# Kernel optimization log

Hardware: AMD Instinct MI355X
Metric: run time of the kernel (lower is better)

## Reference

```python
import jax, jax.numpy as jnp
import numpy as np

B, N, D = 32, 128, 1024


def _euclid_cost(a, b):
    # a: [N, D], b: [N, D] -> [N, N] Euclidean distances (torch.cdist p=2)
    a = a.astype(np.float64)
    b = b.astype(np.float64)
    sq = (a * a).sum(-1)[:, None] + (b * b).sum(-1)[None, :] - 2.0 * (a @ b.T)
    return np.sqrt(np.maximum(sq, 0.0))


def _hungarian(cost):
    """Exact LAP via shortest augmenting path (Kuhn-Munkres with potentials).
    Returns col_for_row: row i is matched to column col_for_row[i].
    Equivalent to scipy.optimize.linear_sum_assignment on a square matrix
    (row_ind == arange(N))."""
    n = cost.shape[0]
    INF = 1e18
    c = cost.astype(np.float64)
    u = np.zeros(n + 1)
    v = np.zeros(n + 1)
    p = np.zeros(n + 1, dtype=np.int64)   # p[j] = row matched to column j (1-based)
    way = np.zeros(n + 1, dtype=np.int64)
    for i in range(1, n + 1):
        p[0] = i
        j0 = 0
        minv = np.full(n + 1, INF)
        used = np.zeros(n + 1, dtype=bool)
        while True:
            used[j0] = True
            i0 = p[j0]
            free = ~used[1:]
            cand = c[i0 - 1] - u[i0] - v[1:]
            better = free & (cand < minv[1:])
            idx = np.nonzero(better)[0]
            minv[idx + 1] = cand[idx]
            way[idx + 1] = j0
            free_j = np.nonzero(free)[0] + 1
            j1 = free_j[np.argmin(minv[free_j])]
            delta = minv[j1]
            u[p[used]] += delta
            v[used] -= delta
            minv[~used] -= delta
            j0 = j1
            if p[j0] == 0:
                break
        while j0:
            j1 = way[j0]
            p[j0] = p[j1]
            j0 = j1
    col_for_row = np.zeros(n, dtype=np.int64)
    for j in range(1, n + 1):
        col_for_row[p[j] - 1] = j - 1
    return col_for_row


def _match(pred_nodes, target_nodes):
    # Host-side exact bipartite matching (mirrors the .cpu() + scipy solve;
    # non-differentiable, indices treated as constants like torch's detach()).
    pn = np.asarray(jax.device_get(pred_nodes))
    tn = np.asarray(jax.device_get(target_nodes))
    cols = [_hungarian(_euclid_cost(pn[b], tn[b])) for b in range(pn.shape[0])]
    return jnp.asarray(np.stack(cols))  # [B, N] int64


def setup_inputs() -> dict:
    key = jax.random.key(0)
    k1, k2, k3, k4 = jax.random.split(key, 4)
    return {
        "pred_nodes": jax.random.normal(k1, (B, N, D), dtype=jnp.float32),
        "target_nodes": jax.random.normal(k2, (B, N, D), dtype=jnp.float32),
        "pred_adj": jax.random.normal(k3, (B, N, N), dtype=jnp.float32),
        "target_adj": jax.random.normal(k4, (B, N, N), dtype=jnp.float32),
    }


def reference(pred_nodes, target_nodes, pred_adj, target_adj):
    col = _match(pred_nodes, target_nodes)  # [B, N]; row_ind is identity
    # matched target nodes: target_nodes[b][col_ind]
    tn_m = jnp.take_along_axis(target_nodes, col[:, :, None], axis=1)  # [B, N, D]
    # nn.MSELoss() = mean over elements per sample; losses summed over batch
    node_loss = jnp.mean((pred_nodes - tn_m) ** 2, axis=(1, 2)).sum()
    # target_adj[b][col_ind][:, col_ind]; pred_adj row_ind gather is identity
    ta_m = jnp.take_along_axis(target_adj, col[:, :, None], axis=1)
    ta_m = jnp.take_along_axis(ta_m, col[:, None, :], axis=2)  # [B, N, N]
    edge_loss = jnp.mean((pred_adj - ta_m) ** 2, axis=(1, 2)).sum()
    return node_loss, edge_loss
```

## Files before the change

kernel.cpp:

```cpp
#include <hip/hip_runtime.h>
#include <hip/hip_bf16.h>
#include <math.h>

#define BB 32
#define NN 128
#define DD 1024
#define INF64 1e30

__global__ __launch_bounds__(128) void cost_kernel(const float* __restrict__ pred,
                                                   const float* __restrict__ tgt,
                                                   double* __restrict__ cost) {
  int blk = blockIdx.x;
  int b = blk >> 4;
  int it = (blk & 15) << 3;
  const float* Ab = pred + ((size_t)b * NN + it) * DD;
  const float* Bb = tgt + (size_t)b * NN * DD;
  __shared__ float a_s[8 * DD];
  for (int t = threadIdx.x; t < 8 * DD / 4; t += 128) {
    ((float4*)a_s)[t] = ((const float4*)Ab)[t];
  }
  __syncthreads();
  const int j = threadIdx.x;
  const float4* brow = (const float4*)(Bb + (size_t)j * DD);
  double acc[8];
#pragma unroll
  for (int r = 0; r < 8; r++) acc[r] = 0.0;
  for (int k4 = 0; k4 < DD / 4; k4++) {
    float4 bv = brow[k4];
#pragma unroll
    for (int r = 0; r < 8; r++) {
      float4 av = ((const float4*)(a_s + r * DD))[k4];
      double d0 = (double)av.x - (double)bv.x;
      double d1 = (double)av.y - (double)bv.y;
      double d2 = (double)av.z - (double)bv.z;
      double d3 = (double)av.w - (double)bv.w;
      acc[r] += d0 * d0 + d1 * d1 + d2 * d2 + d3 * d3;
    }
  }
#pragma unroll
  for (int r = 0; r < 8; r++) {
    cost[(((size_t)b * NN) + it + r) * NN + j] = sqrt(acc[r]);
  }
}

union f64u { double d; unsigned int i[2]; };

__device__ __forceinline__ double readlane_f64(double x, int lane) {
  f64u u; u.d = x;
  f64u v;
  v.i[0] = (unsigned)__builtin_amdgcn_readlane((int)u.i[0], lane);
  v.i[1] = (unsigned)__builtin_amdgcn_readlane((int)u.i[1], lane);
  return v.d;
}

__device__ __forceinline__ double readpair_f64(double a, double b, int idx) {
  int l = (idx - 1) & 63;
  double ra = readlane_f64(a, l);
  double rb = readlane_f64(b, l);
  return ((idx - 1) >> 6) ? rb : ra;
}

__device__ __forceinline__ int readpair_i32(int a, int b, int idx) {
  int l = (idx - 1) & 63;
  int ra = __builtin_amdgcn_readlane(a, l);
  int rb = __builtin_amdgcn_readlane(b, l);
  return ((idx - 1) >> 6) ? rb : ra;
}

__device__ __forceinline__ double pack_key(double m, int idx) {
  unsigned long long bits = __double_as_longlong(fmax(m, 0.0));
  bits = (bits & ~127ull) | (unsigned long long)idx;
  return __longlong_as_double(bits);
}

#define DPP_MIN_STEP(r, CTRL)                                                        \
  do {                                                                               \
    f64u _t; _t.d = (r);                                                             \
    f64u _s;                                                                         \
    _s.i[0] = (unsigned)__builtin_amdgcn_update_dpp((int)_t.i[0], (int)_t.i[0],      \
                                                    (CTRL), 0xF, 0xF, false);        \
    _s.i[1] = (unsigned)__builtin_amdgcn_update_dpp((int)_t.i[1], (int)_t.i[1],      \
                                                    (CTRL), 0xF, 0xF, false);        \
    (r) = fmin((r), _s.d);                                                           \
  } while (0)

__global__ __launch_bounds__(64) void hungarian_kernel(const double* __restrict__ cost,
                                                       int* __restrict__ colfor) {
  extern __shared__ double lds[];
  const int b = blockIdx.x;
  const double* C = cost + (size_t)b * NN * NN;
  const int lane = threadIdx.x;
  const int jA = lane + 1;
  const int jB = lane + 65;

  {
    const double2* src = (const double2*)C;
    double2* dst = (double2*)lds;
#pragma unroll 8
    for (int t = lane; t < NN * NN / 2; t += 64) dst[t] = src[t];
  }
  __syncthreads();

  double vA = INF64, vB = INF64;
  int argA = 0, argB = 0;
#pragma unroll 4
  for (int i = 0; i < NN; i++) {
    double cA = lds[(size_t)i * NN + lane];
    double cB = lds[(size_t)i * NN + lane + 64];
    if (cA < vA) { vA = cA; argA = i + 1; }
    if (cB < vB) { vB = cB; argB = i + 1; }
  }

  unsigned long long asgLo = 0ull, asgHi = 0ull;
  int pA = 0, pB = 0;
  for (int j = 1; j <= NN; j++) {
    int ar = readpair_i32(argA, argB, j);
    bool freeRow = (ar <= 64) ? !((asgLo >> (ar - 1)) & 1ull)
                              : !((asgHi >> (ar - 65)) & 1ull);
    if (freeRow) {
      if (ar <= 64) asgLo |= 1ull << (ar - 1); else asgHi |= 1ull << (ar - 65);
      if (j == jA) pA = ar;
      if (j == jB) pB = ar;
    }
  }

  double uA = 0.0, uB = 0.0;

  for (int i = 1; i <= NN; i++) {
    bool seeded = (i <= 64) ? ((asgLo >> (i - 1)) & 1ull)
                            : ((asgHi >> (i - 65)) & 1ull);
    if (seeded) continue;

    double minvA = INF64, minvB = INF64;
    int wayA = 0, wayB = 0;
    int usedA = 0, usedB = 0;
    unsigned long long usedRowLo = 0ull, usedRowHi = 0ull;
    int j0 = 0;
    int i0 = i;
    int jfin;
    while (true) {
      usedA |= (j0 == jA);
      usedB |= (j0 == jB);
      if (i0 <= 64) usedRowLo |= 1ull << (i0 - 1); else usedRowHi |= 1ull << (i0 - 65);
      double u_i0 = readpair_f64(uA, uB, i0);
      const double* crow = lds + (size_t)(i0 - 1) * NN;
      double cA = crow[lane];
      double cB = crow[lane + 64];
      double candA = cA - u_i0 - vA;
      double candB = cB - u_i0 - vB;
      if (!usedA && candA < minvA) { minvA = candA; wayA = j0; }
      if (!usedB && candB < minvB) { minvB = candB; wayB = j0; }
      double kA = pack_key(usedA ? INF64 : minvA, lane);
      double kB = pack_key(usedB ? INF64 : minvB, lane + 64);
      double r = fmin(kA, kB);
      DPP_MIN_STEP(r, 0x111);
      DPP_MIN_STEP(r, 0x112);
      DPP_MIN_STEP(r, 0x114);
      DPP_MIN_STEP(r, 0x118);
      DPP_MIN_STEP(r, 0x142);
      DPP_MIN_STEP(r, 0x143);
      double rmin = readlane_f64(r, 63);
      unsigned long long bits = __double_as_longlong(rmin);
      int j1 = (int)(bits & 127ull) + 1;
      double delta = __longlong_as_double(bits & ~127ull);
      if ((usedRowLo >> lane) & 1ull) uA += delta;
      if ((usedRowHi >> lane) & 1ull) uB += delta;
      if (usedA) vA -= delta; else minvA -= delta;
      if (usedB) vB -= delta; else minvB -= delta;
      int pj1 = readpair_i32(pA, pB, j1);
      j0 = j1;
      if (pj1 == 0) { jfin = j1; break; }
      i0 = pj1;
    }
    int j = jfin;
    while (j) {
      int wj = readpair_i32(wayA, wayB, j);
      int pn = (wj == 0) ? i : readpair_i32(pA, pB, wj);
      if (j == jA) pA = pn;
      if (j == jB) pB = pn;
      j = wj;
    }
  }
  colfor[b * NN + (pA - 1)] = jA - 1;
  colfor[b * NN + (pB - 1)] = jB - 1;
}

__global__ __launch_bounds__(256) void node_loss_kernel(const float* __restrict__ pred,
                                                        const float* __restrict__ tgt,
                                                        const int* __restrict__ col,
                                                        double* __restrict__ partial) {
  const size_t total = (size_t)BB * NN * (DD / 4);
  double s = 0.0;
  for (size_t idx = (size_t)blockIdx.x * blockDim.x + threadIdx.x; idx < total;
       idx += (size_t)gridDim.x * blockDim.x) {
    size_t k4 = idx & (DD / 4 - 1);
    size_t bi = idx / (DD / 4);
    int i = (int)(bi & (NN - 1));
    int b = (int)(bi >> 7);
    int c = col[b * NN + i];
    float4 pv = ((const float4*)pred)[idx];
    float4 tv = ((const float4*)(tgt + ((size_t)b * NN + c) * DD))[k4];
    float d0 = pv.x - tv.x, d1 = pv.y - tv.y, d2 = pv.z - tv.z, d3 = pv.w - tv.w;
    s += (double)d0 * d0 + (double)d1 * d1 + (double)d2 * d2 + (double)d3 * d3;
  }
  __shared__ double red[256];
  red[threadIdx.x] = s;
  __syncthreads();
  for (int off = 128; off > 0; off >>= 1) {
    if (threadIdx.x < off) red[threadIdx.x] += red[threadIdx.x + off];
    __syncthreads();
  }
  if (threadIdx.x == 0) partial[blockIdx.x] = red[0];
}

__global__ __launch_bounds__(256) void edge_loss_kernel(const float* __restrict__ padj,
                                                        const float* __restrict__ tadj,
                                                        const int* __restrict__ col,
                                                        double* __restrict__ partial) {
  const size_t total = (size_t)BB * NN * NN;
  double s = 0.0;
  for (size_t idx = (size_t)blockIdx.x * blockDim.x + threadIdx.x; idx < total;
       idx += (size_t)gridDim.x * blockDim.x) {
    int j = (int)(idx & (NN - 1));
    size_t bi = idx >> 7;
    int i = (int)(bi & (NN - 1));
    int b = (int)(bi >> 7);
    int ci = col[b * NN + i];
    int cj = col[b * NN + j];
    float diff = padj[idx] - tadj[((size_t)b * NN + ci) * NN + cj];
    s += (double)diff * (double)diff;
  }
  __shared__ double red[256];
  red[threadIdx.x] = s;
  __syncthreads();
  for (int off = 128; off > 0; off >>= 1) {
    if (threadIdx.x < off) red[threadIdx.x] += red[threadIdx.x + off];
    __syncthreads();
  }
  if (threadIdx.x == 0) partial[blockIdx.x] = red[0];
}

__global__ __launch_bounds__(256) void finalize_kernel(const double* __restrict__ nodeP, int nNode,
                                                       const double* __restrict__ edgeP, int nEdge,
                                                       float* __restrict__ out) {
  __shared__ double red[256];
  double s = 0.0;
  for (int t = threadIdx.x; t < nNode; t += 256) s += nodeP[t];
  red[threadIdx.x] = s;
  __syncthreads();
  for (int off = 128; off > 0; off >>= 1) {
    if (threadIdx.x < off) red[threadIdx.x] += red[threadIdx.x + off];
    __syncthreads();
  }
  double nodeSum = red[0];
  __syncthreads();
  s = 0.0;
  for (int t = threadIdx.x; t < nEdge; t += 256) s += edgeP[t];
  red[threadIdx.x] = s;
  __syncthreads();
  for (int off = 128; off > 0; off >>= 1) {
    if (threadIdx.x < off) red[threadIdx.x] += red[threadIdx.x + off];
    __syncthreads();
  }
  if (threadIdx.x == 0) {
    out[0] = (float)(nodeSum / (double)(NN * DD));
    out[1] = (float)(red[0] / (double)(NN * NN));
  }
}

extern "C" void kernel_launch(void* const* d_in, const int* in_sizes, int n_in,
                              void* d_out, int out_size, void* d_ws, size_t ws_size,
                              hipStream_t stream) {
  const float* pred_nodes   = (const float*)d_in[0];
  const float* target_nodes = (const float*)d_in[1];
  const float* pred_adj     = (const float*)d_in[2];
  const float* target_adj   = (const float*)d_in[3];
  float* out = (float*)d_out;

  char* ws = (char*)d_ws;
  double* cost = (double*)ws;
  size_t off = (size_t)BB * NN * NN * sizeof(double);
  int* col = (int*)(ws + off);
  off += (size_t)BB * NN * sizeof(int);
  double* nodeP = (double*)(ws + off);
  double* edgeP = nodeP + 512;

  cost_kernel<<<BB * 16, 128, 0, stream>>>(pred_nodes, target_nodes, cost);
  hungarian_kernel<<<BB, 64, 131072, stream>>>(cost, col);
  node_loss_kernel<<<512, 256, 0, stream>>>(pred_nodes, target_nodes, col, nodeP);
  edge_loss_kernel<<<128, 256, 0, stream>>>(pred_adj, target_adj, col, edgeP);
  finalize_kernel<<<1, 256, 0, stream>>>(nodeP, 512, edgeP, 128, out);
}
```

Measured before the change: 831.9 us.

## Add auction-style augmenting row reduction before shortest-path Hungarian phase

Adds a JV-style augmenting row reduction pass ahead of the shortest augmenting path loop. Each free row finds its best and second-best reduced costs with two DPP min reductions, takes a column, adjusts that column's potential, and can displace the previous owner, which goes back into the free-row set. The pass is capped at 256 steps, and any rows still free are then handled by the existing Dijkstra-style augmentation. The aim is to cut down the number of long augmenting searches, at the cost of two extra wave reductions per step and more complex potential bookkeeping that must keep the result exact.

```diff
diff --git a/kernel.cpp b/kernel.cpp
--- a/kernel.cpp
+++ b/kernel.cpp
@@ -84,6 +84,16 @@
     (r) = fmin((r), _s.d);                                                           \
   } while (0)
 
+#define DPP_MIN_CHAIN(r)          \
+  do {                            \
+    DPP_MIN_STEP(r, 0x111);       \
+    DPP_MIN_STEP(r, 0x112);       \
+    DPP_MIN_STEP(r, 0x114);       \
+    DPP_MIN_STEP(r, 0x118);       \
+    DPP_MIN_STEP(r, 0x142);       \
+    DPP_MIN_STEP(r, 0x143);       \
+  } while (0)
+
 __global__ __launch_bounds__(64) void hungarian_kernel(const double* __restrict__ cost,
                                                        int* __restrict__ colfor) {
   extern __shared__ double lds[];
@@ -126,10 +136,46 @@
 
   double uA = 0.0, uB = 0.0;
 
-  for (int i = 1; i <= NN; i++) {
-    bool seeded = (i <= 64) ? ((asgLo >> (i - 1)) & 1ull)
-                            : ((asgHi >> (i - 65)) & 1ull);
-    if (seeded) continue;
+  unsigned long long mLo = ~asgLo, mHi = ~asgHi;
+  int steps = 0;
+  while ((mLo | mHi) != 0ull && steps < 256) {
+    steps++;
+    int i = mLo ? (__builtin_ctzll(mLo) + 1) : (__builtin_ctzll(mHi) + 65);
+    if (i <= 64) mLo &= ~(1ull << (i - 1)); else mHi &= ~(1ull << (i - 65));
+    const double* crow = lds + (size_t)(i - 1) * NN;
+    double kA = pack_key(crow[lane] - vA, lane);
+    double kB = pack_key(crow[lane + 64] - vB, lane + 64);
+    double r1 = fmin(kA, kB);
+    DPP_MIN_CHAIN(r1);
+    unsigned long long bits1 = __double_as_longlong(readlane_f64(r1, 63));
+    int j1 = (int)(bits1 & 127ull) + 1;
+    double u1 = __longlong_as_double((long long)(bits1 & ~127ull));
+    double r2 = fmin((jA == j1) ? INF64 : kA, (jB == j1) ? INF64 : kB);
+    DPP_MIN_CHAIN(r2);
+    unsigned long long bits2 = __double_as_longlong(readlane_f64(r2, 63));
+    int j2 = (int)(bits2 & 127ull) + 1;
+    double u2 = __longlong_as_double((long long)(bits2 & ~127ull));
+
+    int pj1 = readpair_i32(pA, pB, j1);
+    if (u1 < u2) {
+      if (jA == j1) vA -= (u2 - u1);
+      if (jB == j1) vB -= (u2 - u1);
+    } else if (pj1 != 0) {
+      j1 = j2;
+      pj1 = readpair_i32(pA, pB, j1);
+    }
+    if (jA == j1) pA = i;
+    if (jB == j1) pB = i;
+    if (i <= 64) { if (lane == i - 1) uA = u2; }
+    else         { if (lane == i - 65) uB = u2; }
+    if (pj1 != 0) {
+      if (pj1 <= 64) mLo |= 1ull << (pj1 - 1); else mHi |= 1ull << (pj1 - 65);
+    }
+  }
+
+  while ((mLo | mHi) != 0ull) {
+    int i = mLo ? (__builtin_ctzll(mLo) + 1) : (__builtin_ctzll(mHi) + 65);
+    if (i <= 64) mLo &= ~(1ull << (i - 1)); else mHi &= ~(1ull << (i - 65));
 
     double minvA = INF64, minvB = INF64;
     int wayA = 0, wayB = 0;
@@ -153,16 +199,11 @@
       double kA = pack_key(usedA ? INF64 : minvA, lane);
       double kB = pack_key(usedB ? INF64 : minvB, lane + 64);
       double r = fmin(kA, kB);
-      DPP_MIN_STEP(r, 0x111);
-      DPP_MIN_STEP(r, 0x112);
-      DPP_MIN_STEP(r, 0x114);
-      DPP_MIN_STEP(r, 0x118);
-      DPP_MIN_STEP(r, 0x142);
-      DPP_MIN_STEP(r, 0x143);
+      DPP_MIN_CHAIN(r);
       double rmin = readlane_f64(r, 63);
       unsigned long long bits = __double_as_longlong(rmin);
       int j1 = (int)(bits & 127ull) + 1;
-      double delta = __longlong_as_double(bits & ~127ull);
+      double delta = __longlong_as_double((long long)(bits & ~127ull));
       if ((usedRowLo >> lane) & 1ull) uA += delta;
       if ((usedRowHi >> lane) & 1ull) uB += delta;
       if (usedA) vA -= delta; else minvA -= delta;
```

New measurement: 899.7 us. +8.1%, slower.
